# Optimization experiments

Measured on AMD Instinct MI355X. Metric: run time of the kernel, lower is better.

Reference implementation:

```python
import jax, jax.numpy as jnp
import numpy as np

N_NODES = 50000


def _gcn_layer(x, src, dst, W, b, n_nodes):
    # x: [N, Cin] -> linear -> [N, Cout]
    h = x @ W.T + b
    # degree over destination (col) index, including self loops
    deg = jax.ops.segment_sum(jnp.ones(src.shape[0], dtype=x.dtype), dst,
                              num_segments=n_nodes)
    dinv = jnp.where(deg > 0, deg ** -0.5, jnp.zeros((), x.dtype))
    norm = dinv[src] * dinv[dst]                      # [E]
    msg = h[src] * norm[:, None]                      # gather + scale
    return jax.ops.segment_sum(msg, dst, num_segments=n_nodes)  # scatter-add


def setup_inputs() -> dict:
    key = jax.random.key(0)
    k1, k2, k3, k4, k5, k6 = jax.random.split(key, 6)
    num_features = 128
    hidden_dim = 128
    n_edges = 1_600_000
    x = jax.random.normal(k1, (N_NODES, num_features), dtype=jnp.float32)
    edge_index = jax.random.randint(k2, (2, n_edges), 0, N_NODES, dtype=jnp.int64)
    bound1 = 1.0 / np.sqrt(num_features)
    W1 = jax.random.uniform(k3, (hidden_dim, num_features), jnp.float32, -bound1, bound1)
    b1 = jax.random.uniform(k4, (hidden_dim,), jnp.float32, -bound1, bound1)
    bound2 = 1.0 / np.sqrt(hidden_dim)
    W2 = jax.random.uniform(k5, (hidden_dim, hidden_dim), jnp.float32, -bound2, bound2)
    b2 = jax.random.uniform(k6, (hidden_dim,), jnp.float32, -bound2, bound2)
    return {"x": x, "edge_index": edge_index, "W1": W1, "b1": b1, "W2": W2, "b2": b2}


def reference(x, edge_index, W1, b1, W2, b2):
    n_nodes = x.shape[0]
    # add_self_loops: append (i, i) for every node
    loops = jnp.arange(n_nodes, dtype=edge_index.dtype)
    src = jnp.concatenate([edge_index[0], loops])
    dst = jnp.concatenate([edge_index[1], loops])
    h = _gcn_layer(x, src, dst, W1, b1, n_nodes)
    h = jax.nn.relu(h)
    # dropout is identity in eval mode (deterministic reference)
    out = _gcn_layer(h, src, dst, W2, b2, n_nodes)
    return out
```

## Files before the change

kernel.cpp:

```cpp
#include <hip/hip_runtime.h>


static constexpr int F = 128;
static constexpr int NR = 128;
static constexpr int CH = 2048;
static constexpr int CAP = 4608;
static constexpr int RMAX = 512;

typedef __attribute__((ext_vector_type(8))) short bf16x8;
typedef __attribute__((ext_vector_type(4))) float f32x4;
typedef __attribute__((ext_vector_type(4))) unsigned short u16x4;

__device__ __forceinline__ unsigned f2b(float x) {
  unsigned u = __float_as_uint(x);
  return (u + 0x7fffu + ((u >> 16) & 1u)) >> 16;
}
__device__ __forceinline__ float b_lo(unsigned u) {
  return __uint_as_float(u << 16);
}
__device__ __forceinline__ float b_hi(unsigned u) {
  return __uint_as_float(u & 0xffff0000u);
}

__global__ void k_initcur(int* __restrict__ gcur, int R) {
  int i = blockIdx.x * blockDim.x + threadIdx.x;
  if (i < R) gcur[i] = i * CAP;
}

__global__ __launch_bounds__(512) void k_part(const int* __restrict__ src,
                                              const int* __restrict__ dst,
                                              int E, int R,
                                              int* __restrict__ gcur,
                                              unsigned* __restrict__ rsorted) {
  __shared__ int h[RMAX];
  __shared__ int cur[RMAX];
  const int tid = threadIdx.x;
  for (int i = tid; i < R; i += 512) h[i] = 0;
  __syncthreads();
  const int e0 = blockIdx.x * CH;
  const int idx = e0 + tid * 4;
  int d0 = -1, d1 = -1, d2 = -1, d3 = -1;
  int s0 = 0, s1 = 0, s2 = 0, s3 = 0;
  if (idx + 3 < E) {
    const int4 dv = *(const int4*)(dst + idx);
    const int4 sv = *(const int4*)(src + idx);
    d0 = dv.x; d1 = dv.y; d2 = dv.z; d3 = dv.w;
    s0 = sv.x; s1 = sv.y; s2 = sv.z; s3 = sv.w;
  } else {
    if (idx < E)     { d0 = dst[idx];     s0 = src[idx]; }
    if (idx + 1 < E) { d1 = dst[idx + 1]; s1 = src[idx + 1]; }
    if (idx + 2 < E) { d2 = dst[idx + 2]; s2 = src[idx + 2]; }
    if (idx + 3 < E) { d3 = dst[idx + 3]; s3 = src[idx + 3]; }
  }
  if (d0 >= 0) atomicAdd(&h[d0 >> 7], 1);
  if (d1 >= 0) atomicAdd(&h[d1 >> 7], 1);
  if (d2 >= 0) atomicAdd(&h[d2 >> 7], 1);
  if (d3 >= 0) atomicAdd(&h[d3 >> 7], 1);
  __syncthreads();
  for (int i = tid; i < R; i += 512)
    cur[i] = h[i] ? atomicAdd(&gcur[i], h[i]) : 0;
  __syncthreads();
  if (d0 >= 0) { const int p = atomicAdd(&cur[d0 >> 7], 1); rsorted[p] = ((unsigned)(d0 & (NR - 1)) << 16) | (unsigned)s0; }
  if (d1 >= 0) { const int p = atomicAdd(&cur[d1 >> 7], 1); rsorted[p] = ((unsigned)(d1 & (NR - 1)) << 16) | (unsigned)s1; }
  if (d2 >= 0) { const int p = atomicAdd(&cur[d2 >> 7], 1); rsorted[p] = ((unsigned)(d2 & (NR - 1)) << 16) | (unsigned)s2; }
  if (d3 >= 0) { const int p = atomicAdd(&cur[d3 >> 7], 1); rsorted[p] = ((unsigned)(d3 & (NR - 1)) << 16) | (unsigned)s3; }
}

__global__ __launch_bounds__(512) void k_fillR(
    const unsigned* __restrict__ rsorted, const int* __restrict__ gcur,
    int N, int* __restrict__ rowptr, int* __restrict__ rowend,
    float* __restrict__ dinv, unsigned short* __restrict__ csr) {
  __shared__ unsigned seg[CAP];
  __shared__ int cnt[NR];
  __shared__ int sc[NR];
  __shared__ int cur[NR];
  const int r = blockIdx.x;
  const int tid = threadIdx.x;
  const int b = r * CAP;
  int e = gcur[r];
  if (e > b + CAP) e = b + CAP;
  const int len = e - b;

  if (tid < NR) cnt[tid] = 0;
  __syncthreads();
  for (int i = tid; i < len; i += 512) {
    const unsigned v = rsorted[b + i];
    seg[i] = v;
    atomicAdd(&cnt[v >> 16], 1);
  }
  __syncthreads();
  if (tid < NR) sc[tid] = cnt[tid];
  __syncthreads();
#pragma unroll
  for (int off = 1; off < NR; off <<= 1) {
    const int a = (tid < NR && tid >= off) ? sc[tid - off] : 0;
    __syncthreads();
    if (tid < NR) sc[tid] += a;
    __syncthreads();
  }
  if (tid < NR) {
    const int excl = sc[tid] - cnt[tid];
    cur[tid] = excl;
    const int node = r * NR + tid;
    if (node < N) {
      rowptr[node] = b + excl;
      rowend[node] = b + excl + cnt[tid];
      dinv[node] = rsqrtf((float)(cnt[tid] + 1));
    }
  }
  __syncthreads();
  for (int i = tid; i < len; i += 512) {
    const unsigned v = seg[i];
    const int p = atomicAdd(&cur[v >> 16], 1);
    csr[b + p] = (unsigned short)(v & 0xFFFFu);
  }
}

__global__ __launch_bounds__(256) void k_splitW(
    const float* __restrict__ W1, const float* __restrict__ W2,
    unsigned short* __restrict__ hi1, unsigned short* __restrict__ lo1,
    unsigned short* __restrict__ hi2, unsigned short* __restrict__ lo2) {
  const int bi = blockIdx.x;
  const float* __restrict__ W = (bi < 64) ? W1 : W2;
  unsigned short* __restrict__ hi = (bi < 64) ? hi1 : hi2;
  unsigned short* __restrict__ lo = (bi < 64) ? lo1 : lo2;
  const int i = (bi & 63) * 256 + threadIdx.x;
  const int j = i & 7;
  const int lane = (i >> 3) & 63;
  const int f = (i >> 9) & 7;
  const int t = i >> 12;
  const int col = f * 16 + (lane & 15);
  const int k = t * 32 + ((j & 4) << 2) + 4 * (lane >> 4) + (j & 3);
  const float x = W[col * F + k];
  const unsigned h = f2b(x);
  hi[i] = (unsigned short)h;
  lo[i] = (unsigned short)f2b(x - __uint_as_float(h << 16));
}

template <bool PRESPLIT>
__global__ __launch_bounds__(256) void k_gemm_mfma(
    const float* __restrict__ Af32, const unsigned short* __restrict__ Ahi,
    const unsigned short* __restrict__ Alo,
    const unsigned short* __restrict__ Whi, const unsigned short* __restrict__ Wlo,
    const float* __restrict__ bias, const float* __restrict__ dinv,
    unsigned short* __restrict__ hout, int n) {
  __shared__ unsigned short sWhi[4096];
  __shared__ unsigned short sWlo[4096];
  const int tid = threadIdx.x;
  const int wid = tid >> 6;
  const int lane = tid & 63;
  const int r = lane & 15;
  const int g = lane >> 4;
  const int m0 = blockIdx.x * 64 + wid * 16;
  const int arow = m0 + r;

  f32x4 acc[8];
#pragma unroll
  for (int f = 0; f < 8; ++f) acc[f] = (f32x4){0.f, 0.f, 0.f, 0.f};

  for (int t = 0; t < 4; ++t) {
    __syncthreads();
    {
      const uint4* __restrict__ gh = (const uint4*)(Whi + t * 4096);
      const uint4* __restrict__ gl = (const uint4*)(Wlo + t * 4096);
      uint4* dh = (uint4*)sWhi;
      uint4* dl = (uint4*)sWlo;
      dh[tid] = gh[tid];
      dh[tid + 256] = gh[tid + 256];
      dl[tid] = gl[tid];
      dl[tid + 256] = gl[tid + 256];
    }
    __syncthreads();

    const int kt = t * 32;
    bf16x8 ahi = (bf16x8){0, 0, 0, 0, 0, 0, 0, 0};
    bf16x8 alo = (bf16x8){0, 0, 0, 0, 0, 0, 0, 0};
    if (arow < n) {
      if (PRESPLIT) {
        const size_t ab = (size_t)arow * F + kt + 4 * g;
        const u16x4 h0 = *(const u16x4*)(Ahi + ab);
        const u16x4 h1 = *(const u16x4*)(Ahi + ab + 16);
        const u16x4 l0 = *(const u16x4*)(Alo + ab);
        const u16x4 l1 = *(const u16x4*)(Alo + ab + 16);
        ahi[0] = (short)h0[0]; ahi[1] = (short)h0[1]; ahi[2] = (short)h0[2]; ahi[3] = (short)h0[3];
        ahi[4] = (short)h1[0]; ahi[5] = (short)h1[1]; ahi[6] = (short)h1[2]; ahi[7] = (short)h1[3];
        alo[0] = (short)l0[0]; alo[1] = (short)l0[1]; alo[2] = (short)l0[2]; alo[3] = (short)l0[3];
        alo[4] = (short)l1[0]; alo[5] = (short)l1[1]; alo[6] = (short)l1[2]; alo[7] = (short)l1[3];
      } else {
        const float4 a0 = *(const float4*)(Af32 + (size_t)arow * F + kt + 4 * g);
        const float4 a1 = *(const float4*)(Af32 + (size_t)arow * F + kt + 16 + 4 * g);
        unsigned h;
        h = f2b(a0.x); ahi[0] = (short)h; alo[0] = (short)f2b(a0.x - __uint_as_float(h << 16));
        h = f2b(a0.y); ahi[1] = (short)h; alo[1] = (short)f2b(a0.y - __uint_as_float(h << 16));
        h = f2b(a0.z); ahi[2] = (short)h; alo[2] = (short)f2b(a0.z - __uint_as_float(h << 16));
        h = f2b(a0.w); ahi[3] = (short)h; alo[3] = (short)f2b(a0.w - __uint_as_float(h << 16));
        h = f2b(a1.x); ahi[4] = (short)h; alo[4] = (short)f2b(a1.x - __uint_as_float(h << 16));
        h = f2b(a1.y); ahi[5] = (short)h; alo[5] = (short)f2b(a1.y - __uint_as_float(h << 16));
        h = f2b(a1.z); ahi[6] = (short)h; alo[6] = (short)f2b(a1.z - __uint_as_float(h << 16));
        h = f2b(a1.w); ahi[7] = (short)h; alo[7] = (short)f2b(a1.w - __uint_as_float(h << 16));
      }
    }
#pragma unroll
    for (int f = 0; f < 8; ++f) {
      const bf16x8 bhi = *(const bf16x8*)(sWhi + (f * 64 + lane) * 8);
      const bf16x8 blo = *(const bf16x8*)(sWlo + (f * 64 + lane) * 8);
      acc[f] = __builtin_amdgcn_mfma_f32_16x16x32_bf16(ahi, bhi, acc[f], 0, 0, 0);
      acc[f] = __builtin_amdgcn_mfma_f32_16x16x32_bf16(ahi, blo, acc[f], 0, 0, 0);
      acc[f] = __builtin_amdgcn_mfma_f32_16x16x32_bf16(alo, bhi, acc[f], 0, 0, 0);
    }
  }

  int orow[4];
  float dv[4];
#pragma unroll
  for (int j = 0; j < 4; ++j) {
    orow[j] = m0 + 4 * g + j;
    dv[j] = (orow[j] < n) ? dinv[orow[j]] : 0.f;
  }
#pragma unroll
  for (int f = 0; f < 8; ++f) {
    const int col = f * 16 + r;
    const float bv = bias[col];
#pragma unroll
    for (int j = 0; j < 4; ++j) {
      if (orow[j] < n)
        hout[(size_t)orow[j] * F + col] = (unsigned short)f2b((acc[f][j] + bv) * dv[j]);
    }
  }
}

template <int MODE>
__global__ __launch_bounds__(256) void k_pull(
    const int* __restrict__ rowptr, const int* __restrict__ rowend,
    const unsigned short* __restrict__ csr, const uint2* __restrict__ h,
    const float* __restrict__ dinv, unsigned short* __restrict__ ahi,
    unsigned short* __restrict__ alo, float* __restrict__ fout, int n) {
  const int wid = (blockIdx.x * blockDim.x + threadIdx.x) >> 6;
  if (wid >= n) return;
  const int lane = threadIdx.x & 63;
  const int half = lane >> 5;
  const int l32 = lane & 31;
  const int beg = rowptr[wid];
  const int end = rowend[wid];

  float4 acc = make_float4(0.f, 0.f, 0.f, 0.f);
  if (half == 0) {
    const uint2 u = h[(size_t)wid * 32 + l32];
    acc.x = b_lo(u.x); acc.y = b_hi(u.x);
    acc.z = b_lo(u.y); acc.w = b_hi(u.y);
  }

  int k = beg + half;
  for (; k + 6 < end; k += 8) {
    const int s0 = csr[k];
    const int s1 = csr[k + 2];
    const int s2 = csr[k + 4];
    const int s3 = csr[k + 6];
    const uint2 u0 = h[(size_t)s0 * 32 + l32];
    const uint2 u1 = h[(size_t)s1 * 32 + l32];
    const uint2 u2 = h[(size_t)s2 * 32 + l32];
    const uint2 u3 = h[(size_t)s3 * 32 + l32];
    acc.x += b_lo(u0.x) + b_lo(u1.x) + b_lo(u2.x) + b_lo(u3.x);
    acc.y += b_hi(u0.x) + b_hi(u1.x) + b_hi(u2.x) + b_hi(u3.x);
    acc.z += b_lo(u0.y) + b_lo(u1.y) + b_lo(u2.y) + b_lo(u3.y);
    acc.w += b_hi(u0.y) + b_hi(u1.y) + b_hi(u2.y) + b_hi(u3.y);
  }
  for (; k < end; k += 2) {
    const uint2 u = h[(size_t)csr[k] * 32 + l32];
    acc.x += b_lo(u.x);
    acc.y += b_hi(u.x);
    acc.z += b_lo(u.y);
    acc.w += b_hi(u.y);
  }

  acc.x += __shfl_xor(acc.x, 32, 64);
  acc.y += __shfl_xor(acc.y, 32, 64);
  acc.z += __shfl_xor(acc.z, 32, 64);
  acc.w += __shfl_xor(acc.w, 32, 64);

  if (half == 0) {
    const float dv = dinv[wid];
    float rx = acc.x * dv;
    float ry = acc.y * dv;
    float rz = acc.z * dv;
    float rw = acc.w * dv;
    if (MODE == 0) {
      rx = fmaxf(rx, 0.f);
      ry = fmaxf(ry, 0.f);
      rz = fmaxf(rz, 0.f);
      rw = fmaxf(rw, 0.f);
      u16x4 hv, lv;
      unsigned u;
      u = f2b(rx); hv[0] = (unsigned short)u; lv[0] = (unsigned short)f2b(rx - __uint_as_float(u << 16));
      u = f2b(ry); hv[1] = (unsigned short)u; lv[1] = (unsigned short)f2b(ry - __uint_as_float(u << 16));
      u = f2b(rz); hv[2] = (unsigned short)u; lv[2] = (unsigned short)f2b(rz - __uint_as_float(u << 16));
      u = f2b(rw); hv[3] = (unsigned short)u; lv[3] = (unsigned short)f2b(rw - __uint_as_float(u << 16));
      *(u16x4*)(ahi + (size_t)wid * F + l32 * 4) = hv;
      *(u16x4*)(alo + (size_t)wid * F + l32 * 4) = lv;
    } else {
      float4 rv;
      rv.x = rx; rv.y = ry; rv.z = rz; rv.w = rw;
      *(float4*)(fout + (size_t)wid * F + l32 * 4) = rv;
    }
  }
}

extern "C" void kernel_launch(void* const* d_in, const int* in_sizes, int n_in,
                              void* d_out, int out_size, void* d_ws, size_t ws_size,
                              hipStream_t stream) {
  const float* x  = (const float*)d_in[0];
  const int*   ei = (const int*)d_in[1];
  const float* W1 = (const float*)d_in[2];
  const float* b1 = (const float*)d_in[3];
  const float* W2 = (const float*)d_in[4];
  const float* b2 = (const float*)d_in[5];

  const int N = in_sizes[0] / F;
  const int E = in_sizes[1] / 2;
  const int* src = ei;
  const int* dst = ei + E;
  const int R = (N + NR - 1) / NR;
  const int C = (E + CH - 1) / CH;

  char* ws = (char*)d_ws;
  int*            gcur    = (int*)(ws + (8u << 10));
  float*          dinv    = (float*)(ws + (16u << 10));
  int*            rowptr  = (int*)(ws + (256u << 10));
  int*            rowend  = (int*)(ws + (512u << 10));
  unsigned short* Whi1    = (unsigned short*)(ws + (768u << 10));
  unsigned short* Wlo1    = (unsigned short*)(ws + (800u << 10));
  unsigned short* Whi2    = (unsigned short*)(ws + (832u << 10));
  unsigned short* Wlo2    = (unsigned short*)(ws + (864u << 10));
  unsigned*       rsorted = (unsigned*)(ws + (1u << 20));
  unsigned short* csr     = (unsigned short*)(ws + (9u << 20));
  unsigned short* hbuf    = (unsigned short*)(ws + (16u << 20));
  unsigned short* Ahi     = (unsigned short*)(ws + (32u << 20));
  unsigned short* Alo     = (unsigned short*)(ws + (45u << 20));
  float*          out     = (float*)d_out;

  const int B = 256;
  const int gemmBlocks = (N + 63) / 64;
  const int pullBlocks = (N * 64 + B - 1) / B;

  k_initcur<<<(R + 255) / 256, B, 0, stream>>>(gcur, R);
  k_part<<<C, 512, 0, stream>>>(src, dst, E, R, gcur, rsorted);
  k_fillR<<<R, 512, 0, stream>>>(rsorted, gcur, N, rowptr, rowend, dinv, csr);
  k_splitW<<<128, B, 0, stream>>>(W1, W2, Whi1, Wlo1, Whi2, Wlo2);

  k_gemm_mfma<false><<<gemmBlocks, B, 0, stream>>>(x, nullptr, nullptr, Whi1,
                                                   Wlo1, b1, dinv, hbuf, N);
  k_pull<0><<<pullBlocks, B, 0, stream>>>(rowptr, rowend, csr,
                                          (const uint2*)hbuf, dinv, Ahi, Alo,
                                          nullptr, N);

  k_gemm_mfma<true><<<gemmBlocks, B, 0, stream>>>(nullptr, Ahi, Alo, Whi2,
                                                  Wlo2, b2, dinv, hbuf, N);
  k_pull<1><<<pullBlocks, B, 0, stream>>>(rowptr, rowend, csr,
                                          (const uint2*)hbuf, dinv, nullptr,
                                          nullptr, out, N);
}
```

Measured before the change: 191.0 us.

## Persist GEMM blocks with full W in LDS and fold gcur init into splitW

The GEMM kernel now loads the whole split weight matrix (hi and lo, 64 KB) into shared memory once per block. It then loops over row tiles in a grid-stride persistent fashion with 512 blocks, which removes the per-k-step weight reloads and barriers. Separately, the gcur initialisation kernel is merged into k_splitW, saving one launch. The larger LDS footprint lowers occupancy per CU, and the fixed grid of 512 blocks may leave the ~782 tiles unevenly distributed.

```diff
diff --git a/kernel.cpp b/kernel.cpp
--- a/kernel.cpp
+++ b/kernel.cpp
@@ -20,11 +20,6 @@
 }
 __device__ __forceinline__ float b_hi(unsigned u) {
   return __uint_as_float(u & 0xffff0000u);
-}
-
-__global__ void k_initcur(int* __restrict__ gcur, int R) {
-  int i = blockIdx.x * blockDim.x + threadIdx.x;
-  if (i < R) gcur[i] = i * CAP;
 }
 
 __global__ __launch_bounds__(512) void k_part(const int* __restrict__ src,
@@ -119,8 +114,11 @@
 __global__ __launch_bounds__(256) void k_splitW(
     const float* __restrict__ W1, const float* __restrict__ W2,
     unsigned short* __restrict__ hi1, unsigned short* __restrict__ lo1,
-    unsigned short* __restrict__ hi2, unsigned short* __restrict__ lo2) {
+    unsigned short* __restrict__ hi2, unsigned short* __restrict__ lo2,
+    int* __restrict__ gcur, int R) {
   const int bi = blockIdx.x;
+  const int gi = bi * 256 + threadIdx.x;
+  if (gi < R) gcur[gi] = gi * CAP;
   const float* __restrict__ W = (bi < 64) ? W1 : W2;
   unsigned short* __restrict__ hi = (bi < 64) ? hi1 : hi2;
   unsigned short* __restrict__ lo = (bi < 64) ? lo1 : lo2;
@@ -143,88 +141,92 @@
     const unsigned short* __restrict__ Alo,
     const unsigned short* __restrict__ Whi, const unsigned short* __restrict__ Wlo,
     const float* __restrict__ bias, const float* __restrict__ dinv,
-    unsigned short* __restrict__ hout, int n) {
-  __shared__ unsigned short sWhi[4096];
-  __shared__ unsigned short sWlo[4096];
+    unsigned short* __restrict__ hout, int n, int nTiles) {
+  __shared__ unsigned short sWhi[16384];
+  __shared__ unsigned short sWlo[16384];
   const int tid = threadIdx.x;
+  {
+    const uint4* __restrict__ gh = (const uint4*)Whi;
+    const uint4* __restrict__ gl = (const uint4*)Wlo;
+    uint4* dh = (uint4*)sWhi;
+    uint4* dl = (uint4*)sWlo;
+#pragma unroll
+    for (int i = 0; i < 8; ++i) {
+      dh[tid + i * 256] = gh[tid + i * 256];
+      dl[tid + i * 256] = gl[tid + i * 256];
+    }
+  }
+  __syncthreads();
+
   const int wid = tid >> 6;
   const int lane = tid & 63;
   const int r = lane & 15;
   const int g = lane >> 4;
-  const int m0 = blockIdx.x * 64 + wid * 16;
-  const int arow = m0 + r;
-
-  f32x4 acc[8];
-#pragma unroll
-  for (int f = 0; f < 8; ++f) acc[f] = (f32x4){0.f, 0.f, 0.f, 0.f};
-
-  for (int t = 0; t < 4; ++t) {
-    __syncthreads();
-    {
-      const uint4* __restrict__ gh = (const uint4*)(Whi + t * 4096);
-      const uint4* __restrict__ gl = (const uint4*)(Wlo + t * 4096);
-      uint4* dh = (uint4*)sWhi;
-      uint4* dl = (uint4*)sWlo;
-      dh[tid] = gh[tid];
-      dh[tid + 256] = gh[tid + 256];
-      dl[tid] = gl[tid];
-      dl[tid + 256] = gl[tid + 256];
-    }
-    __syncthreads();
-
-    const int kt = t * 32;
-    bf16x8 ahi = (bf16x8){0, 0, 0, 0, 0, 0, 0, 0};
-    bf16x8 alo = (bf16x8){0, 0, 0, 0, 0, 0, 0, 0};
-    if (arow < n) {
-      if (PRESPLIT) {
-        const size_t ab = (size_t)arow * F + kt + 4 * g;
-        const u16x4 h0 = *(const u16x4*)(Ahi + ab);
-        const u16x4 h1 = *(const u16x4*)(Ahi + ab + 16);
-        const u16x4 l0 = *(const u16x4*)(Alo + ab);
-        const u16x4 l1 = *(const u16x4*)(Alo + ab + 16);
-        ahi[0] = (short)h0[0]; ahi[1] = (short)h0[1]; ahi[2] = (short)h0[2]; ahi[3] = (short)h0[3];
-        ahi[4] = (short)h1[0]; ahi[5] = (short)h1[1]; ahi[6] = (short)h1[2]; ahi[7] = (short)h1[3];
-        alo[0] = (short)l0[0]; alo[1] = (short)l0[1]; alo[2] = (short)l0[2]; alo[3] = (short)l0[3];
-        alo[4] = (short)l1[0]; alo[5] = (short)l1[1]; alo[6] = (short)l1[2]; alo[7] = (short)l1[3];
-      } else {
-        const float4 a0 = *(const float4*)(Af32 + (size_t)arow * F + kt + 4 * g);
-        const float4 a1 = *(const float4*)(Af32 + (size_t)arow * F + kt + 16 + 4 * g);
-        unsigned h;
-        h = f2b(a0.x); ahi[0] = (short)h; alo[0] = (short)f2b(a0.x - __uint_as_float(h << 16));
-        h = f2b(a0.y); ahi[1] = (short)h; alo[1] = (short)f2b(a0.y - __uint_as_float(h << 16));
-        h = f2b(a0.z); ahi[2] = (short)h; alo[2] = (short)f2b(a0.z - __uint_as_float(h << 16));
-        h = f2b(a0.w); ahi[3] = (short)h; alo[3] = (short)f2b(a0.w - __uint_as_float(h << 16));
-        h = f2b(a1.x); ahi[4] = (short)h; alo[4] = (short)f2b(a1.x - __uint_as_float(h << 16));
-        h = f2b(a1.y); ahi[5] = (short)h; alo[5] = (short)f2b(a1.y - __uint_as_float(h << 16));
-        h = f2b(a1.z); ahi[6] = (short)h; alo[6] = (short)f2b(a1.z - __uint_as_float(h << 16));
-        h = f2b(a1.w); ahi[7] = (short)h; alo[7] = (short)f2b(a1.w - __uint_as_float(h << 16));
+
+  for (int bt = blockIdx.x; bt < nTiles; bt += gridDim.x) {
+    const int m0 = bt * 64 + wid * 16;
+    const int arow = m0 + r;
+
+    f32x4 acc[8];
+#pragma unroll
+    for (int f = 0; f < 8; ++f) acc[f] = (f32x4){0.f, 0.f, 0.f, 0.f};
+
+#pragma unroll
+    for (int t = 0; t < 4; ++t) {
+      const int kt = t * 32;
+      bf16x8 ahi = (bf16x8){0, 0, 0, 0, 0, 0, 0, 0};
+      bf16x8 alo = (bf16x8){0, 0, 0, 0, 0, 0, 0, 0};
+      if (arow < n) {
+        if (PRESPLIT) {
+          const size_t ab = (size_t)arow * F + kt + 4 * g;
+          const u16x4 h0 = *(const u16x4*)(Ahi + ab);
+          const u16x4 h1 = *(const u16x4*)(Ahi + ab + 16);
+          const u16x4 l0 = *(const u16x4*)(Alo + ab);
+          const u16x4 l1 = *(const u16x4*)(Alo + ab + 16);
+          ahi[0] = (short)h0[0]; ahi[1] = (short)h0[1]; ahi[2] = (short)h0[2]; ahi[3] = (short)h0[3];
+          ahi[4] = (short)h1[0]; ahi[5] = (short)h1[1]; ahi[6] = (short)h1[2]; ahi[7] = (short)h1[3];
+          alo[0] = (short)l0[0]; alo[1] = (short)l0[1]; alo[2] = (short)l0[2]; alo[3] = (short)l0[3];
+          alo[4] = (short)l1[0]; alo[5] = (short)l1[1]; alo[6] = (short)l1[2]; alo[7] = (short)l1[3];
+        } else {
+          const float4 a0 = *(const float4*)(Af32 + (size_t)arow * F + kt + 4 * g);
+          const float4 a1 = *(const float4*)(Af32 + (size_t)arow * F + kt + 16 + 4 * g);
+          unsigned h;
+          h = f2b(a0.x); ahi[0] = (short)h; alo[0] = (short)f2b(a0.x - __uint_as_float(h << 16));
+          h = f2b(a0.y); ahi[1] = (short)h; alo[1] = (short)f2b(a0.y - __uint_as_float(h << 16));
+          h = f2b(a0.z); ahi[2] = (short)h; alo[2] = (short)f2b(a0.z - __uint_as_float(h << 16));
+          h = f2b(a0.w); ahi[3] = (short)h; alo[3] = (short)f2b(a0.w - __uint_as_float(h << 16));
+          h = f2b(a1.x); ahi[4] = (short)h; alo[4] = (short)f2b(a1.x - __uint_as_float(h << 16));
+          h = f2b(a1.y); ahi[5] = (short)h; alo[5] = (short)f2b(a1.y - __uint_as_float(h << 16));
+          h = f2b(a1.z); ahi[6] = (short)h; alo[6] = (short)f2b(a1.z - __uint_as_float(h << 16));
+          h = f2b(a1.w); ahi[7] = (short)h; alo[7] = (short)f2b(a1.w - __uint_as_float(h << 16));
+        }
       }
+#pragma unroll
+      for (int f = 0; f < 8; ++f) {
+        const bf16x8 bhi = *(const bf16x8*)(sWhi + ((t * 8 + f) * 64 + lane) * 8);
+        const bf16x8 blo = *(const bf16x8*)(sWlo + ((t * 8 + f) * 64 + lane) * 8);
+        acc[f] = __builtin_amdgcn_mfma_f32_16x16x32_bf16(ahi, bhi, acc[f], 0, 0, 0);
+        acc[f] = __builtin_amdgcn_mfma_f32_16x16x32_bf16(ahi, blo, acc[f], 0, 0, 0);
+        acc[f] = __builtin_amdgcn_mfma_f32_16x16x32_bf16(alo, bhi, acc[f], 0, 0, 0);
+      }
+    }
+
+    int orow[4];
+    float dv[4];
+#pragma unroll
+    for (int j = 0; j < 4; ++j) {
+      orow[j] = m0 + 4 * g + j;
+      dv[j] = (orow[j] < n) ? dinv[orow[j]] : 0.f;
     }
 #pragma unroll
     for (int f = 0; f < 8; ++f) {
-      const bf16x8 bhi = *(const bf16x8*)(sWhi + (f * 64 + lane) * 8);
-      const bf16x8 blo = *(const bf16x8*)(sWlo + (f * 64 + lane) * 8);
-      acc[f] = __builtin_amdgcn_mfma_f32_16x16x32_bf16(ahi, bhi, acc[f], 0, 0, 0);
-      acc[f] = __builtin_amdgcn_mfma_f32_16x16x32_bf16(ahi, blo, acc[f], 0, 0, 0);
-      acc[f] = __builtin_amdgcn_mfma_f32_16x16x32_bf16(alo, bhi, acc[f], 0, 0, 0);
-    }
-  }
-
-  int orow[4];
-  float dv[4];
-#pragma unroll
-  for (int j = 0; j < 4; ++j) {
-    orow[j] = m0 + 4 * g + j;
-    dv[j] = (orow[j] < n) ? dinv[orow[j]] : 0.f;
-  }
-#pragma unroll
-  for (int f = 0; f < 8; ++f) {
-    const int col = f * 16 + r;
-    const float bv = bias[col];
-#pragma unroll
-    for (int j = 0; j < 4; ++j) {
-      if (orow[j] < n)
-        hout[(size_t)orow[j] * F + col] = (unsigned short)f2b((acc[f][j] + bv) * dv[j]);
+      const int col = f * 16 + r;
+      const float bv = bias[col];
+#pragma unroll
+      for (int j = 0; j < 4; ++j) {
+        if (orow[j] < n)
+          hout[(size_t)orow[j] * F + col] = (unsigned short)f2b((acc[f][j] + bv) * dv[j]);
+      }
     }
   }
 }
@@ -339,22 +341,24 @@
   float*          out     = (float*)d_out;
 
   const int B = 256;
-  const int gemmBlocks = (N + 63) / 64;
+  const int nTiles = (N + 63) / 64;
+  const int gemmBlocks = 512;
   const int pullBlocks = (N * 64 + B - 1) / B;
 
-  k_initcur<<<(R + 255) / 256, B, 0, stream>>>(gcur, R);
+  k_splitW<<<128, B, 0, stream>>>(W1, W2, Whi1, Wlo1, Whi2, Wlo2, gcur, R);
   k_part<<<C, 512, 0, stream>>>(src, dst, E, R, gcur, rsorted);
   k_fillR<<<R, 512, 0, stream>>>(rsorted, gcur, N, rowptr, rowend, dinv, csr);
-  k_splitW<<<128, B, 0, stream>>>(W1, W2, Whi1, Wlo1, Whi2, Wlo2);
 
   k_gemm_mfma<false><<<gemmBlocks, B, 0, stream>>>(x, nullptr, nullptr, Whi1,
-                                                   Wlo1, b1, dinv, hbuf, N);
+                                                   Wlo1, b1, dinv, hbuf, N,
+                                                   nTiles);
   k_pull<0><<<pullBlocks, B, 0, stream>>>(rowptr, rowend, csr,
                                           (const uint2*)hbuf, dinv, Ahi, Alo,
                                           nullptr, N);
 
   k_gemm_mfma<true><<<gemmBlocks, B, 0, stream>>>(nullptr, Ahi, Alo, Whi2,
-                                                  Wlo2, b2, dinv, hbuf, N);
+                                                  Wlo2, b2, dinv, hbuf, N,
+                                                  nTiles);
   k_pull<1><<<pullBlocks, B, 0, stream>>>(rowptr, rowend, csr,
                                           (const uint2*)hbuf, dinv, nullptr,
                                           nullptr, out, N);
```

New measurement: 214.3 us. 12.2% more time.
